# Optimization experiments

Hardware: AMD Instinct MI355X
Metric: run time of the kernel (lower is better)

## Reference

```python
import jax, jax.numpy as jnp
import numpy as np

RESO = 64
PAD = 0.1
SCALE = 8.0
PLANES = {'xz': (0, 2), 'xy': (0, 1), 'yz': (1, 2)}
PLANE_ORDER = ['xz', 'xy', 'yz']


def normalize_coordinate(p, plane):
    i, j = PLANES[plane]
    xy = jnp.stack([p[..., i], p[..., j]], axis=-1)
    xy = xy / (1.0 + PAD + 1e-3) + 0.5
    return jnp.clip(xy, 0.0, 1.0 - 1e-5)


def coordinate2index(xy, reso):
    x = (xy * reso).astype(jnp.int32)
    return x[..., 0] + reso * x[..., 1]  # (B, T)


def resblock(x, W0, b0, W1, b1, Ws):
    # ResnetBlockFC: fc_1(relu(fc_0(relu(x)))) + shortcut(x)
    net = jnp.maximum(x, 0.0) @ W0 + b0
    dx = jnp.maximum(net, 0.0) @ W1 + b1
    return x @ Ws + dx


def scatter_max_pool(c, idx_flat, num_seg):
    # c: (B, T, h); idx_flat: (B*T,) batch-offset plane indices
    B, T, h = c.shape
    pooled = jax.ops.segment_max(c.reshape(B * T, h), idx_flat, num_segments=num_seg)
    return pooled[idx_flat].reshape(B, T, h)


def plane_feature(p, c, plane):
    # scatter_mean of c into (B, c_dim, RESO, RESO); empty cells -> 0
    B, T, cd = c.shape
    R2 = RESO * RESO
    idx = coordinate2index(normalize_coordinate(p / SCALE, plane), RESO)
    idxf = (idx + jnp.arange(B, dtype=jnp.int32)[:, None] * R2).reshape(-1)
    sums = jax.ops.segment_sum(c.reshape(B * T, cd), idxf, num_segments=B * R2)
    cnt = jax.ops.segment_sum(jnp.ones((B * T,), c.dtype), idxf, num_segments=B * R2)
    mean = sums / jnp.maximum(cnt, 1.0)[:, None]
    return mean.reshape(B, R2, cd).transpose(0, 2, 1).reshape(B, cd, RESO, RESO)


def forward(p, fc_pos_W, fc_pos_b, blocks_W0, blocks_b0, blocks_W1, blocks_b1, blocks_Ws, fc_c_W, fc_c_b):
    B, T, _ = p.shape
    R2 = RESO * RESO
    offs = jnp.arange(B, dtype=jnp.int32)[:, None] * R2
    idx = {k: (coordinate2index(normalize_coordinate(p / SCALE, k), RESO) + offs).reshape(-1)
           for k in PLANE_ORDER}

    net = p @ fc_pos_W + fc_pos_b  # (B, T, 3h)
    net = resblock(net, blocks_W0[0], blocks_b0[0], blocks_W1[0], blocks_b1[0], blocks_Ws[0])
    n_blocks = blocks_W0.shape[0]
    for i in range(1, n_blocks):
        pooled = sum(scatter_max_pool(net, idx[k], B * R2) for k in PLANE_ORDER)
        meanp = jnp.broadcast_to(net.mean(axis=1, keepdims=True), net.shape)
        net = jnp.concatenate([net, pooled, meanp], axis=-1)  # (B, T, 3h)
        net = resblock(net, blocks_W0[i], blocks_b0[i], blocks_W1[i], blocks_b1[i], blocks_Ws[i])

    c = net @ fc_c_W + fc_c_b  # (B, T, c_dim)
    fea = jnp.stack([plane_feature(p, c, k) for k in PLANE_ORDER], axis=0)
    return fea  # (3, B, c_dim, RESO, RESO) in order xz, xy, yz


def setup_inputs() -> dict:
    key = jax.random.key(0)
    ks = jax.random.split(key, 10)
    B, T, dim = 16, 8192, 3
    h, c_dim, nb = 128, 128, 5
    s = 0.05
    return {
        'p': jax.random.normal(ks[0], (B, T, dim), jnp.float32) * 2.0,
        'fc_pos_W': jax.random.normal(ks[1], (dim, 3 * h), jnp.float32) * s,
        'fc_pos_b': jnp.zeros((3 * h,), jnp.float32),
        'blocks_W0': jax.random.normal(ks[2], (nb, 3 * h, h), jnp.float32) * s,
        'blocks_b0': jnp.zeros((nb, h), jnp.float32),
        'blocks_W1': jax.random.normal(ks[3], (nb, h, h), jnp.float32) * s,
        'blocks_b1': jnp.zeros((nb, h), jnp.float32),
        'blocks_Ws': jax.random.normal(ks[4], (nb, 3 * h, h), jnp.float32) * s,
        'fc_c_W': jax.random.normal(ks[5], (h, c_dim), jnp.float32) * s,
        'fc_c_b': jnp.zeros((c_dim,), jnp.float32),
    }


def reference(p, fc_pos_W, fc_pos_b, blocks_W0, blocks_b0, blocks_W1, blocks_b1, blocks_Ws, fc_c_W, fc_c_b):
    return forward(p, fc_pos_W, fc_pos_b, blocks_W0, blocks_b0, blocks_W1, blocks_b1, blocks_Ws, fc_c_W, fc_c_b)
```

## Files before the change

### kernel.cpp

```cpp
#include <hip/hip_runtime.h>

#define BT (16 * 8192)
#define NB 5
#define NCELL 65536
typedef unsigned int uint;
typedef unsigned short ushort;
typedef __attribute__((ext_vector_type(8))) _Float16 half8;
typedef __attribute__((ext_vector_type(2))) __fp16 fp16x2;
typedef __attribute__((ext_vector_type(2))) _Float16 half2v;
typedef __attribute__((ext_vector_type(4))) float f32x4;


__device__ __forceinline__ uint f2h2(float a, float b) {
    fp16x2 h = __builtin_amdgcn_cvt_pkrtz(a, b);
    return *(uint*)&h;
}
__device__ __forceinline__ float h2f_lo(uint u) { half2v h = *(half2v*)&u; return (float)h[0]; }
__device__ __forceinline__ float h2f_hi(uint u) { half2v h = *(half2v*)&u; return (float)h[1]; }
__device__ __forceinline__ uint pk_add(uint a, uint b) {
    uint d; asm("v_pk_add_f16 %0, %1, %2" : "=v"(d) : "v"(a), "v"(b)); return d;
}
__device__ __forceinline__ uint pk_max(uint a, uint b) {
    uint d; asm("v_pk_max_f16 %0, %1, %2" : "=v"(d) : "v"(a), "v"(b)); return d;
}

__device__ __forceinline__ uint relu2(uint u) {
    uint m = (u >> 15) & 0x00010001u;
    return u & ~(m * 0xffffu);
}
__device__ __forceinline__ half8 relu8(half8 a) {
    uint4 u = *(uint4*)&a;
    u.x = relu2(u.x); u.y = relu2(u.y); u.z = relu2(u.z); u.w = relu2(u.w);
    return *(half8*)&u;
}
__device__ __forceinline__ f32x4 bcast4(float x) { return (f32x4){x, x, x, x}; }
__device__ __forceinline__ f32x4 mfma16(half8 a, half8 b, f32x4 c) {
    return __builtin_amdgcn_mfma_f32_16x16x32_f16(a, b, c, 0, 0, 0);
}

__global__ void k_idx(const float* __restrict__ p, int* __restrict__ idx,
                      int4* __restrict__ idx4) {
    int r = blockIdx.x * 256 + threadIdx.x;
    if (r >= BT) return;
    float p0 = p[3 * r + 0], p1 = p[3 * r + 1], p2 = p[3 * r + 2];
    const float DEN = (float)(1.0 + 0.1 + 1e-3);
    const float HI  = (float)(1.0 - 1e-5);
    int b = r >> 13;
    float x0 = fminf(fmaxf((p0 / 8.0f) / DEN + 0.5f, 0.0f), HI);
    float x1 = fminf(fmaxf((p1 / 8.0f) / DEN + 0.5f, 0.0f), HI);
    float x2 = fminf(fmaxf((p2 / 8.0f) / DEN + 0.5f, 0.0f), HI);
    int i0 = (int)(x0 * 64.0f);
    int i1 = (int)(x1 * 64.0f);
    int i2 = (int)(x2 * 64.0f);
    int base = b << 12;
    int exz = base + i0 + (i2 << 6);
    int exy = base + i0 + (i1 << 6);
    int eyz = base + i1 + (i2 << 6);
    idx[r] = exz; idx[BT + r] = exy; idx[2 * BT + r] = eyz;
    idx4[r] = make_int4(exz, exy, eyz, 0);
}

__global__ void k_hist(const int* __restrict__ idx, int* __restrict__ cnt) {
    int r = blockIdx.x * 256 + threadIdx.x;
    if (r >= BT) return;
    atomicAdd(cnt + idx[r], 1);
    atomicAdd(cnt + NCELL + idx[BT + r], 1);
    atomicAdd(cnt + 2 * NCELL + idx[2 * BT + r], 1);
}

__global__ __launch_bounds__(1024) void k_scan(const int* __restrict__ cnt,
                                               int* __restrict__ starts,
                                               int* __restrict__ cursor) {
    __shared__ int sc[1024];
    int pl = blockIdx.x, t = threadIdx.x;
    const int* c = cnt + pl * NCELL;
    int base = t * 64;
    int s = 0;
    for (int i = 0; i < 64; ++i) s += c[base + i];
    sc[t] = s;
    __syncthreads();
    for (int off = 1; off < 1024; off <<= 1) {
        int v = (t >= off) ? sc[t - off] : 0;
        __syncthreads();
        sc[t] += v;
        __syncthreads();
    }
    int run = sc[t] - s;
    for (int i = 0; i < 64; ++i) {
        int cell = base + i;
        starts[pl * NCELL + cell] = run;
        cursor[pl * NCELL + cell] = run;
        run += c[cell];
    }
}

__global__ void k_scatter_order(const int* __restrict__ idx, int* __restrict__ cursor,
                                int* __restrict__ order) {
    int r = blockIdx.x * 256 + threadIdx.x;
    if (r >= BT) return;
    for (int pl = 0; pl < 3; ++pl) {
        int cell = idx[pl * BT + r];
        int pos = atomicAdd(cursor + pl * NCELL + cell, 1);
        order[pl * BT + pos] = r;
    }
}

__global__ void k_wconv(const float* __restrict__ W0, const float* __restrict__ W1,
                        const float* __restrict__ Ws, const float* __restrict__ Wc,
                        ushort* __restrict__ wb) {
    int mat = blockIdx.y;
    int K = (mat < 5 || (mat >= 10 && mat < 15)) ? 384 : 128;
    int e = blockIdx.x * 256 + threadIdx.x;
    if (e >= K * 128) return;
    const float* src;
    size_t doff;
    if (mat < 5)       { src = W0 + (size_t)mat * 49152;        doff = (size_t)mat * 49152; }
    else if (mat < 10) { src = W1 + (size_t)(mat - 5) * 16384;  doff = 245760 + (size_t)(mat - 5) * 16384; }
    else if (mat < 15) { src = Ws + (size_t)(mat - 10) * 49152; doff = 327680 + (size_t)(mat - 10) * 49152; }
    else               { src = Wc;                              doff = 573440; }
    int ko = e & 31, n = (e >> 5) & 127, kt = e >> 12;
    wb[doff + e] = (ushort)f2h2(src[(size_t)(kt * 32 + ko) * 128 + n], 0.0f);
}

__global__ __launch_bounds__(256) void k_segmax(const uint* __restrict__ netu,
                                                const int* __restrict__ starts,
                                                const int* __restrict__ cnt,
                                                const int* __restrict__ order,
                                                uint* __restrict__ segu,
                                                const float* __restrict__ meanPrev,
                                                const ushort* __restrict__ wb0,
                                                const float* __restrict__ b0v,
                                                const ushort* __restrict__ wbs,
                                                const float* __restrict__ b1v,
                                                float* __restrict__ rv0,
                                                float* __restrict__ rvS) {
    int t = threadIdx.x;
    if (blockIdx.x >= 49152) {
        __shared__ float ms[128];
        int b = blockIdx.x - 49152;
        if (t < 128) ms[t] = meanPrev[b * 128 + t];
        __syncthreads();
        if (t < 128) {
            float s0 = b0v[t], ss = b1v[t];
#pragma unroll 4
            for (int k = 0; k < 128; ++k) {
                float mv = ms[k];
                int kt = 8 + (k >> 5), ko = k & 31;
                float w0 = h2f_lo((uint)wb0[kt * 4096 + t * 32 + ko]);
                float ws = h2f_lo((uint)wbs[kt * 4096 + t * 32 + ko]);
                s0 = fmaf(fmaxf(mv, 0.0f), w0, s0);
                ss = fmaf(mv, ws, ss);
            }
            rv0[b * 128 + t] = s0;
            rvS[b * 128 + t] = ss;
        }
        return;
    }
    int g = blockIdx.x * 4 + (t >> 6);
    int l = t & 63;
    int n = cnt[g];
    if (n == 0) return;
    int pl = g >> 16;
    const int* ord = order + pl * BT + starts[g];
    uint m = 0xFC00FC00u;
    int i = 0;
    for (; i + 4 <= n; i += 4) {
        uint a = netu[(size_t)ord[i] * 64 + l];
        uint b = netu[(size_t)ord[i + 1] * 64 + l];
        uint c = netu[(size_t)ord[i + 2] * 64 + l];
        uint d = netu[(size_t)ord[i + 3] * 64 + l];
        m = pk_max(m, pk_max(pk_max(a, b), pk_max(c, d)));
    }
    int rem = n - i;
    if (rem > 0) {
        uint a = netu[(size_t)ord[i] * 64 + l];
        uint b = (rem > 1) ? netu[(size_t)ord[i + 1] * 64 + l] : a;
        uint c = (rem > 2) ? netu[(size_t)ord[i + 2] * 64 + l] : a;
        m = pk_max(m, pk_max(a, pk_max(b, c)));
    }
    segu[(size_t)g * 64 + l] = m;
}

template <int MODE>
__global__ __launch_bounds__(512, MODE == 0 ? 6 : 8) void k_resblock(
    const float* __restrict__ p, const uint* __restrict__ netu,
    const int4* __restrict__ idx4, const ushort* __restrict__ seg,
    const float* __restrict__ rv0, const float* __restrict__ rvS,
    const float* __restrict__ Wp, const float* __restrict__ bp,
    const ushort* __restrict__ wb0, const float* __restrict__ b0v,
    const ushort* __restrict__ wb1, const float* __restrict__ b1v,
    const ushort* __restrict__ wbs,
    ushort* __restrict__ out, float* __restrict__ meanW) {
    constexpr int LDA = (MODE == 0) ? 392 : 264;
    constexpr int NKT = (MODE == 0) ? 12 : 8;
    __shared__ __align__(16) ushort aT[64 * LDA];
    ushort* hT = aT;
    const int t = threadIdx.x;
    const int rowBase = blockIdx.x * 64;
    const int bb = rowBase >> 13;

    if constexpr (MODE == 0) {
        for (int f = t; f < 3072; f += 512) {
            int row = f / 48, g = f - row * 48;
            const float* pr = p + (size_t)(rowBase + row) * 3;
            float p0 = pr[0], p1 = pr[1], p2 = pr[2];
            int k0 = g * 8;
            uint d[4];
#pragma unroll
            for (int w = 0; w < 4; ++w) {
                int k = k0 + 2 * w;
                float v0 = bp[k]     + p0 * Wp[k]     + p1 * Wp[384 + k]     + p2 * Wp[768 + k];
                float v1 = bp[k + 1] + p0 * Wp[k + 1] + p1 * Wp[384 + k + 1] + p2 * Wp[768 + k + 1];
                d[w] = f2h2(v0, v1);
            }
            *(uint4*)(aT + row * LDA + k0) = make_uint4(d[0], d[1], d[2], d[3]);
        }
    } else {
        const uint4* nsrc = (const uint4*)netu;
#pragma unroll
        for (int i = 0; i < 2; ++i) {
            int f = t + 512 * i;
            int row = f >> 4, cu = f & 15;
            *(uint4*)(aT + row * LDA + cu * 8) = nsrc[(size_t)(rowBase + row) * 16 + cu];
        }
#pragma unroll
        for (int i = 0; i < 2; ++i) {
            int f = t + 512 * i;
            int row = f >> 4, grp = f & 15;
            int4 cc = idx4[rowBase + row];
            uint4 A = *(const uint4*)(seg + ((size_t)cc.x) * 128 + grp * 8);
            uint4 B = *(const uint4*)(seg + ((size_t)NCELL + cc.y) * 128 + grp * 8);
            uint4 C = *(const uint4*)(seg + ((size_t)2 * NCELL + cc.z) * 128 + grp * 8);
            uint4 d;
            d.x = pk_add(pk_add(A.x, B.x), C.x);
            d.y = pk_add(pk_add(A.y, B.y), C.y);
            d.z = pk_add(pk_add(A.z, B.z), C.z);
            d.w = pk_add(pk_add(A.w, B.w), C.w);
            *(uint4*)(aT + row * LDA + 128 + grp * 8) = d;
        }
    }
    __syncthreads();

    const int l = t & 63, wid = t >> 6;
    const int n0 = wid * 16;
    const int lm = l & 15, lg = l >> 4;
    const ushort* w0 = wb0 + n0 * 32;
    const ushort* w1 = wb1 + n0 * 32;
    const ushort* ws = wbs + n0 * 32;

    f32x4 acc0[4], accS[4];
    {
        float bi, si;
        if constexpr (MODE == 0) { bi = b0v[n0 + lm];            si = b1v[n0 + lm]; }
        else                     { bi = rv0[bb * 128 + n0 + lm]; si = rvS[bb * 128 + n0 + lm]; }
#pragma unroll
        for (int im = 0; im < 4; ++im) { acc0[im] = bcast4(bi); accS[im] = bcast4(si); }
    }
#pragma unroll
    for (int kt = 0; kt < NKT; ++kt) {
        half8 b0 = *(const half8*)(w0 + kt * 4096 + lm * 32 + lg * 8);
        half8 bs = *(const half8*)(ws + kt * 4096 + lm * 32 + lg * 8);
#pragma unroll
        for (int im = 0; im < 4; ++im) {
            half8 a = *(const half8*)(aT + (im * 16 + lm) * LDA + kt * 32 + lg * 8);
            acc0[im] = mfma16(relu8(a), b0, acc0[im]);
            accS[im] = mfma16(a, bs, accS[im]);
        }
    }
    __syncthreads();

#pragma unroll
    for (int im = 0; im < 4; ++im)
#pragma unroll
        for (int j = 0; j < 4; ++j) {
            int row = im * 16 + lg * 4 + j;
            hT[row * 136 + n0 + lm] = (ushort)f2h2(fmaxf(acc0[im][j], 0.0f), 0.0f);
        }
    __syncthreads();

#pragma unroll
    for (int kt = 0; kt < 4; ++kt) {
        half8 b = *(const half8*)(w1 + kt * 4096 + lm * 32 + lg * 8);
#pragma unroll
        for (int im = 0; im < 4; ++im) {
            half8 a = *(const half8*)(hT + (im * 16 + lm) * 136 + kt * 32 + lg * 8);
            accS[im] = mfma16(a, b, accS[im]);
        }
    }

#pragma unroll
    for (int im = 0; im < 4; ++im)
#pragma unroll
        for (int j = 0; j < 4; ++j) {
            int row = rowBase + im * 16 + lg * 4 + j;
            out[(size_t)row * 128 + n0 + lm] = (ushort)f2h2(accS[im][j], 0.0f);
        }

    if (meanW) {
        float s = 0.0f;
#pragma unroll
        for (int im = 0; im < 4; ++im)
#pragma unroll
            for (int j = 0; j < 4; ++j) s += accS[im][j];
        s += __shfl_xor(s, 16);
        s += __shfl_xor(s, 32);
        if (l < 16) atomicAdd(meanW + bb * 128 + n0 + l, s * (1.0f / 8192.0f));
    }
}

__device__ __forceinline__ void mfma_gemm3(const ushort* __restrict__ aLDS, int lda, int nk,
                                           const ushort* __restrict__ wb, int lm, int lg,
                                           f32x4 acc[4][2]) {
    for (int kt = 0; kt < nk; ++kt) {
        half8 b0 = *(const half8*)(wb + kt * 4096 + lm * 32 + lg * 8);
        half8 b1 = *(const half8*)(wb + kt * 4096 + (16 + lm) * 32 + lg * 8);
#pragma unroll
        for (int im = 0; im < 4; ++im) {
            half8 a = *(const half8*)(aLDS + (im * 16 + lm) * lda + kt * 32 + lg * 8);
            acc[im][0] = mfma16(a, b0, acc[im][0]);
            acc[im][1] = mfma16(a, b1, acc[im][1]);
        }
    }
}

__global__ __launch_bounds__(256, 2) void k_fcc(const uint* __restrict__ netu,
                                                const ushort* __restrict__ wbc,
                                                const float* __restrict__ bc,
                                                ushort* __restrict__ cout) {
    __shared__ __align__(16) ushort aT[64 * 136];
    const int t = threadIdx.x;
    const int rowBase = blockIdx.x * 64;
    const uint4* nsrc = (const uint4*)netu;
#pragma unroll
    for (int i = 0; i < 4; ++i) {
        int u = t + 256 * i;
        int row = u >> 4, cu = u & 15;
        *(uint4*)(aT + row * 136 + cu * 8) = nsrc[(size_t)(rowBase + row) * 16 + cu];
    }
    __syncthreads();
    const int l = t & 63, wid = t >> 6;
    const int n0 = wid * 32;
    const int lm = l & 15, lg = l >> 4;
    f32x4 acc[4][2];
    {
        float ci0 = bc[n0 + lm], ci1 = bc[n0 + 16 + lm];
#pragma unroll
        for (int im = 0; im < 4; ++im) { acc[im][0] = bcast4(ci0); acc[im][1] = bcast4(ci1); }
    }
    mfma_gemm3(aT, 136, 4, wbc + n0 * 32, lm, lg, acc);
#pragma unroll
    for (int im = 0; im < 4; ++im)
#pragma unroll
        for (int ic = 0; ic < 2; ++ic)
#pragma unroll
            for (int j = 0; j < 4; ++j) {
                int row = rowBase + im * 16 + lg * 4 + j;
                int col = n0 + ic * 16 + lm;
                cout[(size_t)row * 128 + col] = (ushort)f2h2(acc[im][ic][j], 0.0f);
            }
}

__global__ __launch_bounds__(256) void k_segfin(const uint* __restrict__ cp,
                                                const int* __restrict__ starts,
                                                const int* __restrict__ cnt,
                                                const int* __restrict__ order,
                                                float* __restrict__ out) {
    __shared__ float tile[64 * 130];
    const int t = threadIdx.x;
    const int w = t >> 6, l = t & 63;
    const int bx = blockIdx.x;
    const int pl = bx >> 10;
    const int rem = bx & 1023;
    const int b = rem >> 6;
    const int cl0 = (rem & 63) << 6;
    const int gbase = pl * NCELL + (b << 12) + cl0;
    const int* ordp = order + pl * BT;

    for (int i = 0; i < 16; ++i) {
        int cellLocal = w * 16 + i;
        int g = gbase + cellLocal;
        int n = cnt[g];
        float s0 = 0.f, s1 = 0.f;
        if (n > 0) {
            const int* ord = ordp + starts[g];
            int j = 0;
            for (; j + 4 <= n; j += 4) {
                uint a = cp[(size_t)ord[j] * 64 + l];
                uint bq = cp[(size_t)ord[j + 1] * 64 + l];
                uint c = cp[(size_t)ord[j + 2] * 64 + l];
                uint d = cp[(size_t)ord[j + 3] * 64 + l];
                s0 += (h2f_lo(a) + h2f_lo(bq)) + (h2f_lo(c) + h2f_lo(d));
                s1 += (h2f_hi(a) + h2f_hi(bq)) + (h2f_hi(c) + h2f_hi(d));
            }
            int rm = n - j;
            if (rm > 0) {
                uint a = cp[(size_t)ord[j] * 64 + l];
                uint bq = (rm > 1) ? cp[(size_t)ord[j + 1] * 64 + l] : 0u;
                uint c = (rm > 2) ? cp[(size_t)ord[j + 2] * 64 + l] : 0u;
                s0 += h2f_lo(a) + (h2f_lo(bq) + h2f_lo(c));
                s1 += h2f_hi(a) + (h2f_hi(bq) + h2f_hi(c));
            }
        }
        *(float2*)(tile + cellLocal * 130 + 2 * l) = make_float2(s0, s1);
    }
    __syncthreads();

    int cn = cnt[gbase + l];
    float inv = cn > 0 ? 1.0f / (float)cn : 0.0f;
    size_t obase = (((size_t)((pl * 16 + b) * 128)) << 12) + cl0 + l;
#pragma unroll 8
    for (int j = 0; j < 32; ++j) {
        int ch = w * 32 + j;
        out[obase + ((size_t)ch << 12)] = tile[l * 130 + ch] * inv;
    }
}

extern "C" void kernel_launch(void* const* d_in, const int* in_sizes, int n_in,
                              void* d_out, int out_size, void* d_ws, size_t ws_size,
                              hipStream_t stream) {
    const float* p  = (const float*)d_in[0];
    const float* Wp = (const float*)d_in[1];
    const float* bp = (const float*)d_in[2];
    const float* W0 = (const float*)d_in[3];
    const float* b0 = (const float*)d_in[4];
    const float* W1 = (const float*)d_in[5];
    const float* b1 = (const float*)d_in[6];
    const float* Ws = (const float*)d_in[7];
    const float* Wc = (const float*)d_in[8];
    const float* bc = (const float*)d_in[9];
    float* out = (float*)d_out;

    ushort* net    = (ushort*)d_ws;
    ushort* seg    = net + 16777216;
    ushort* wb     = seg + 25165824;
    int*    idx    = (int*)(wb + 589824);
    int*    order  = idx + 393216;
    int*    cnt    = order + 393216;
    int*    starts = cnt + 196608;
    int*    cursor = starts + 196608;
    float*  meanB  = (float*)(cursor + 196608);
    float*  rv0    = meanB + 4 * 2048;
    float*  rvS    = rv0 + 2048;
    int4*   idx4   = (int4*)(rvS + 2048);

    k_idx<<<512, 256, 0, stream>>>(p, idx, idx4);
    (void)hipMemsetAsync(cnt, 0, 3 * NCELL * 4, stream);
    k_hist<<<512, 256, 0, stream>>>(idx, cnt);
    k_scan<<<3, 1024, 0, stream>>>(cnt, starts, cursor);
    k_scatter_order<<<512, 256, 0, stream>>>(idx, cursor, order);
    k_wconv<<<dim3(192, 16), 256, 0, stream>>>(W0, W1, Ws, Wc, wb);
    (void)hipMemsetAsync(meanB, 0, 4 * 2048 * 4, stream);

    k_resblock<0><<<2048, 512, 0, stream>>>(
        p, nullptr, nullptr, nullptr, nullptr, nullptr, Wp, bp,
        wb, b0, wb + 245760, b1, wb + 327680, net, meanB);

    for (int i = 1; i < NB; ++i) {
        const ushort* wb0i = wb + (size_t)i * 49152;
        const ushort* wb1i = wb + 245760 + (size_t)i * 16384;
        const ushort* wbsi = wb + 327680 + (size_t)i * 49152;
        k_segmax<<<49168, 256, 0, stream>>>((const uint*)net, starts, cnt, order, (uint*)seg,
                                            meanB + (i - 1) * 2048, wb0i, b0 + i * 128,
                                            wbsi, b1 + i * 128, rv0, rvS);
        float* mw = (i < NB - 1) ? meanB + i * 2048 : nullptr;
        k_resblock<1><<<2048, 512, 0, stream>>>(
            nullptr, (const uint*)net, idx4, seg, rv0, rvS, nullptr, nullptr,
            wb0i, nullptr, wb1i, nullptr, wbsi, net, mw);
    }

    k_fcc<<<2048, 256, 0, stream>>>((const uint*)net, wb + 573440, bc, net);

    k_segfin<<<3072, 256, 0, stream>>>((const uint*)net, starts, cnt, order, out);
}
```

Measured before the change: 756.2 us.

## Scatter fc_c output into per-plane cell-sorted order for contiguous segment reads

The scatter-order pass now also records each point's rank within its cell for every plane. The fc_c kernel writes each output row three times, once per plane, at its sorted position, so the final segment-mean kernel reads contiguous rows instead of gathering through the order array. This trades random gather reads for scattered writes of three times the data. It also needs a larger workspace, with the c3 buffer aliased onto the seg buffer.

Result: faster. 734.6 us, median of 2 (-2.9%).

```diff
diff --git a/kernel.cpp b/kernel.cpp
--- a/kernel.cpp
+++ b/kernel.cpp
@@ -95,13 +95,14 @@
 }
 
 __global__ void k_scatter_order(const int* __restrict__ idx, int* __restrict__ cursor,
-                                int* __restrict__ order) {
+                                int* __restrict__ order, int* __restrict__ rank) {
     int r = blockIdx.x * 256 + threadIdx.x;
     if (r >= BT) return;
     for (int pl = 0; pl < 3; ++pl) {
         int cell = idx[pl * BT + r];
         int pos = atomicAdd(cursor + pl * NCELL + cell, 1);
         order[pl * BT + pos] = r;
+        rank[pl * BT + r] = pos;
     }
 }
 
@@ -324,12 +325,18 @@
 }
 
 __global__ __launch_bounds__(256, 2) void k_fcc(const uint* __restrict__ netu,
+                                                const int* __restrict__ rank,
                                                 const ushort* __restrict__ wbc,
                                                 const float* __restrict__ bc,
-                                                ushort* __restrict__ cout) {
+                                                ushort* __restrict__ c3) {
     __shared__ __align__(16) ushort aT[64 * 136];
+    __shared__ int rkS[3][64];
     const int t = threadIdx.x;
     const int rowBase = blockIdx.x * 64;
+    if (t < 192) {
+        int pl = t >> 6, rr = t & 63;
+        rkS[pl][rr] = rank[pl * BT + rowBase + rr];
+    }
     const uint4* nsrc = (const uint4*)netu;
 #pragma unroll
     for (int i = 0; i < 4; ++i) {
@@ -354,16 +361,18 @@
         for (int ic = 0; ic < 2; ++ic)
 #pragma unroll
             for (int j = 0; j < 4; ++j) {
-                int row = rowBase + im * 16 + lg * 4 + j;
+                int row = im * 16 + lg * 4 + j;
                 int col = n0 + ic * 16 + lm;
-                cout[(size_t)row * 128 + col] = (ushort)f2h2(acc[im][ic][j], 0.0f);
+                ushort v = (ushort)f2h2(acc[im][ic][j], 0.0f);
+                c3[(size_t)rkS[0][row] * 128 + col] = v;
+                c3[((size_t)BT + rkS[1][row]) * 128 + col] = v;
+                c3[((size_t)2 * BT + rkS[2][row]) * 128 + col] = v;
             }
 }
 
-__global__ __launch_bounds__(256) void k_segfin(const uint* __restrict__ cp,
+__global__ __launch_bounds__(256) void k_segfin(const uint* __restrict__ c3,
                                                 const int* __restrict__ starts,
                                                 const int* __restrict__ cnt,
-                                                const int* __restrict__ order,
                                                 float* __restrict__ out) {
     __shared__ float tile[64 * 130];
     const int t = threadIdx.x;
@@ -374,7 +383,6 @@
     const int b = rem >> 6;
     const int cl0 = (rem & 63) << 6;
     const int gbase = pl * NCELL + (b << 12) + cl0;
-    const int* ordp = order + pl * BT;
 
     for (int i = 0; i < 16; ++i) {
         int cellLocal = w * 16 + i;
@@ -382,21 +390,21 @@
         int n = cnt[g];
         float s0 = 0.f, s1 = 0.f;
         if (n > 0) {
-            const int* ord = ordp + starts[g];
+            size_t rowb = (size_t)pl * BT + starts[g];
             int j = 0;
             for (; j + 4 <= n; j += 4) {
-                uint a = cp[(size_t)ord[j] * 64 + l];
-                uint bq = cp[(size_t)ord[j + 1] * 64 + l];
-                uint c = cp[(size_t)ord[j + 2] * 64 + l];
-                uint d = cp[(size_t)ord[j + 3] * 64 + l];
+                uint a = c3[(rowb + j) * 64 + l];
+                uint bq = c3[(rowb + j + 1) * 64 + l];
+                uint c = c3[(rowb + j + 2) * 64 + l];
+                uint d = c3[(rowb + j + 3) * 64 + l];
                 s0 += (h2f_lo(a) + h2f_lo(bq)) + (h2f_lo(c) + h2f_lo(d));
                 s1 += (h2f_hi(a) + h2f_hi(bq)) + (h2f_hi(c) + h2f_hi(d));
             }
             int rm = n - j;
             if (rm > 0) {
-                uint a = cp[(size_t)ord[j] * 64 + l];
-                uint bq = (rm > 1) ? cp[(size_t)ord[j + 1] * 64 + l] : 0u;
-                uint c = (rm > 2) ? cp[(size_t)ord[j + 2] * 64 + l] : 0u;
+                uint a = c3[(rowb + j) * 64 + l];
+                uint bq = (rm > 1) ? c3[(rowb + j + 1) * 64 + l] : 0u;
+                uint c = (rm > 2) ? c3[(rowb + j + 2) * 64 + l] : 0u;
                 s0 += h2f_lo(a) + (h2f_lo(bq) + h2f_lo(c));
                 s1 += h2f_hi(a) + (h2f_hi(bq) + h2f_hi(c));
             }
@@ -430,24 +438,26 @@
     const float* bc = (const float*)d_in[9];
     float* out = (float*)d_out;
 
-    ushort* net    = (ushort*)d_ws;
-    ushort* seg    = net + 16777216;
-    ushort* wb     = seg + 25165824;
+    ushort* c3     = (ushort*)d_ws;
+    ushort* seg    = c3;
+    ushort* net    = c3 + 50331648;
+    ushort* wb     = net + 16777216;
     int*    idx    = (int*)(wb + 589824);
     int*    order  = idx + 393216;
-    int*    cnt    = order + 393216;
+    int*    rank   = order + 393216;
+    int*    cnt    = rank + 393216;
     int*    starts = cnt + 196608;
     int*    cursor = starts + 196608;
-    float*  meanB  = (float*)(cursor + 196608);
+    int4*   idx4   = (int4*)(cursor + 196608);
+    float*  meanB  = (float*)(idx4 + 131072);
     float*  rv0    = meanB + 4 * 2048;
     float*  rvS    = rv0 + 2048;
-    int4*   idx4   = (int4*)(rvS + 2048);
 
     k_idx<<<512, 256, 0, stream>>>(p, idx, idx4);
     (void)hipMemsetAsync(cnt, 0, 3 * NCELL * 4, stream);
     k_hist<<<512, 256, 0, stream>>>(idx, cnt);
     k_scan<<<3, 1024, 0, stream>>>(cnt, starts, cursor);
-    k_scatter_order<<<512, 256, 0, stream>>>(idx, cursor, order);
+    k_scatter_order<<<512, 256, 0, stream>>>(idx, cursor, order, rank);
     k_wconv<<<dim3(192, 16), 256, 0, stream>>>(W0, W1, Ws, Wc, wb);
     (void)hipMemsetAsync(meanB, 0, 4 * 2048 * 4, stream);
 
@@ -468,7 +478,7 @@
             wb0i, nullptr, wb1i, nullptr, wbsi, net, mw);
     }
 
-    k_fcc<<<2048, 256, 0, stream>>>((const uint*)net, wb + 573440, bc, net);
-
-    k_segfin<<<3072, 256, 0, stream>>>((const uint*)net, starts, cnt, order, out);
-}
+    k_fcc<<<2048, 256, 0, stream>>>((const uint*)net, rank, wb + 573440, bc, c3);
+
+    k_segfin<<<3072, 256, 0, stream>>>((const uint*)c3, starts, cnt, out);
+}
```
